# Optimization experiments

Measured on AMD Instinct MI355X. Metric: run time of the kernel, lower is better.

Reference implementation:

```python
import jax, jax.numpy as jnp
import numpy as np

SH_C0 = 0.28209479177387814
EPS2D = 0.3      # gsplat low-pass filter added to 2D covariance diagonal
NEAR = 0.01
ALPHA_MIN = 1.0 / 255.0
ALPHA_MAX = 0.999


def setup_inputs() -> dict:
    key = jax.random.key(0)
    ks = jax.random.split(key, 5)
    N = 2048
    means = 0.1 * jax.random.normal(ks[0], (N, 3), jnp.float32)
    quats = jax.random.normal(ks[1], (N, 4), jnp.float32)
    scales = -2.3 + 0.3 * jax.random.normal(ks[2], (N, 3), jnp.float32)
    opacities = -1.0 + 0.5 * jax.random.normal(ks[3], (N,), jnp.float32)
    sh_coeffs = jax.random.normal(ks[4], (N, 1, 3), jnp.float32)
    viewmats = jnp.eye(4, dtype=jnp.float32).at[2, 3].set(2.0)[None]  # [1,4,4] world->cam
    Ks = jnp.array([[[150.0, 0.0, 64.0], [0.0, 150.0, 64.0], [0.0, 0.0, 1.0]]], jnp.float32)
    return dict(means=means, quats=quats, scales=scales, opacities=opacities,
                sh_coeffs=sh_coeffs, viewmats=viewmats, Ks=Ks, width=128, height=128)


def _splat_render(means, quats, scales, opacities, sh_coeffs, viewmats, Ks, width, height):
    # --- parameter activations (GaussianSplat.activated_parameters) ---
    quats = quats / jnp.linalg.norm(quats, axis=-1, keepdims=True)
    scales = jnp.minimum(jnp.exp(scales), 10.0)
    opac = jax.nn.sigmoid(opacities)                                  # [N]
    colors = jnp.maximum(sh_coeffs[:, 0, :] * SH_C0 + 0.5, 0.0)       # [N,3] sh_degree=0

    # --- 3D covariance from quaternion (w,x,y,z) and scale ---
    w, x, y, z = quats[:, 0], quats[:, 1], quats[:, 2], quats[:, 3]
    R = jnp.stack([
        1 - 2 * (y * y + z * z), 2 * (x * y - w * z), 2 * (x * z + w * y),
        2 * (x * y + w * z), 1 - 2 * (x * x + z * z), 2 * (y * z - w * x),
        2 * (x * z - w * y), 2 * (y * z + w * x), 1 - 2 * (x * x + y * y)],
        axis=-1).reshape(-1, 3, 3)                                    # [N,3,3]
    M = R * scales[:, None, :]                                        # R @ diag(s)
    cov3d = jnp.einsum('nij,nkj->nik', M, M)                          # [N,3,3]

    # --- project to camera frame ---
    Rcw = viewmats[:, :3, :3]                                         # [C,3,3]
    tcw = viewmats[:, :3, 3]                                          # [C,3]
    p_cam = jnp.einsum('cij,nj->cni', Rcw, means) + tcw[:, None, :]   # [C,N,3]
    Vc = jnp.einsum('cij,njk,clk->cnil', Rcw, cov3d, Rcw)             # [C,N,3,3]

    xc, yc, zc = p_cam[..., 0], p_cam[..., 1], p_cam[..., 2]
    valid = zc > NEAR
    zs = jnp.where(valid, zc, 1.0)
    rz = 1.0 / zs
    fx = Ks[:, 0, 0][:, None]; fy = Ks[:, 1, 1][:, None]
    cx = Ks[:, 0, 2][:, None]; cy = Ks[:, 1, 2][:, None]
    u = fx * xc * rz + cx                                             # [C,N]
    v = fy * yc * rz + cy

    # --- EWA 2D covariance: J Vc J^T + eps2d*I, J = d(proj)/d(p_cam) ---
    J00 = fx * rz; J02 = -fx * xc * rz * rz
    J11 = fy * rz; J12 = -fy * yc * rz * rz
    V00, V01, V02 = Vc[..., 0, 0], Vc[..., 0, 1], Vc[..., 0, 2]
    V11, V12, V22 = Vc[..., 1, 1], Vc[..., 1, 2], Vc[..., 2, 2]
    a = J00 * J00 * V00 + 2 * J00 * J02 * V02 + J02 * J02 * V22 + EPS2D
    b = J00 * (J11 * V01 + J12 * V02) + J02 * (J11 * V12 + J12 * V22)
    c = J11 * J11 * V11 + 2 * J11 * J12 * V12 + J12 * J12 * V22 + EPS2D
    det = a * c - b * b
    valid = valid & (det > 0)
    det_s = jnp.where(valid, det, 1.0)
    conA = c / det_s; conB = -b / det_s; conC = a / det_s             # conic (inverse cov)

    # --- per-pixel gaussian evaluation (pixel centers at +0.5) ---
    px = jnp.arange(width, dtype=jnp.float32) + 0.5                   # [W]
    py = jnp.arange(height, dtype=jnp.float32) + 0.5                  # [H]
    dx = px[None, None, :] - u[..., None]                             # [C,N,W]
    dy = py[None, None, :] - v[..., None]                             # [C,N,H]
    sigma = (0.5 * (conA[..., None, None] * (dx * dx)[:, :, None, :]
                    + conC[..., None, None] * (dy * dy)[..., None])
             + conB[..., None, None] * dy[..., None] * dx[:, :, None, :])  # [C,N,H,W]
    alpha = opac[None, :, None, None] * jnp.exp(-sigma)
    alpha = jnp.minimum(alpha, ALPHA_MAX)
    alpha = jnp.where(valid[..., None, None] & (alpha >= ALPHA_MIN), alpha, 0.0)

    # --- front-to-back alpha compositing in depth order ---
    order = jnp.argsort(jnp.where(valid, zc, jnp.inf), axis=1)        # [C,N]
    alpha_s = jnp.take_along_axis(alpha, order[:, :, None, None], axis=1)
    colors_s = jnp.take_along_axis(jnp.broadcast_to(colors[None], (alpha.shape[0],) + colors.shape),
                                   order[:, :, None], axis=1)         # [C,N,3]
    logT = jnp.cumsum(jnp.log1p(-alpha_s), axis=1)
    logT_excl = jnp.pad(logT, ((0, 0), (1, 0), (0, 0), (0, 0)))[:, :-1]
    weights = alpha_s * jnp.exp(logT_excl)                            # [C,N,H,W]
    img = jnp.einsum('cnhw,cnk->chwk', weights, colors_s)             # [C,H,W,3]
    return img


def reference(means, quats, scales, opacities, sh_coeffs, viewmats, Ks, width, height):
    return _splat_render(means, quats, scales, opacities, sh_coeffs, viewmats, Ks, width, height)
```

## Files before the change

kernel.cpp:

```cpp
#include <hip/hip_runtime.h>
#include <math.h>

#define SH_C0     0.28209479177387814f
#define EPS2D     0.3f
#define NEARZ     0.01f
#define ALPHA_MIN (1.0f/255.0f)
#define ALPHA_MAX 0.999f
#define LOG2E     1.4426950408889634f

#define NSEG   16
#define MAXN   2048

__global__ __launch_bounds__(256) void prep_rank_kernel(
        const float* __restrict__ means,
        const float* __restrict__ quats,
        const float* __restrict__ scales,
        const float* __restrict__ opacities,
        const float* __restrict__ sh,
        const float* __restrict__ vm,
        const float* __restrict__ K,
        float* __restrict__ rec,
        float* __restrict__ bbox,
        int N) {
    int wave = blockIdx.x * 4 + (threadIdx.x >> 6);
    int lane = threadIdx.x & 63;
    if (wave >= N) return;
    int i = wave;

    float r00=vm[0], r01=vm[1], r02=vm[2],  t0=vm[3];
    float r10=vm[4], r11=vm[5], r12=vm[6],  t1=vm[7];
    float r20=vm[8], r21=vm[9], r22=vm[10], t2=vm[11];

    float mx = means[3*i+0], my = means[3*i+1], mz = means[3*i+2];
    float zci = r20*mx + r21*my + r22*mz + t2;
    float keyi = (zci > NEARZ) ? zci : INFINITY;
    int cnt = 0;
    for (int j = lane; j < N; j += 64) {
        float ax = means[3*j+0], ay = means[3*j+1], az = means[3*j+2];
        float zcj = r20*ax + r21*ay + r22*az + t2;
        float keyj = (zcj > NEARZ) ? zcj : INFINITY;
        cnt += (keyj < keyi) || (keyj == keyi && j < i);
    }
    #pragma unroll
    for (int off = 32; off > 0; off >>= 1)
        cnt += __shfl_xor(cnt, off, 64);

    float qw = quats[4*i+0], qx = quats[4*i+1], qy = quats[4*i+2], qz = quats[4*i+3];
    float rqn = rsqrtf(qw*qw + qx*qx + qy*qy + qz*qz);
    qw *= rqn; qx *= rqn; qy *= rqn; qz *= rqn;

    float R00 = 1.f - 2.f*(qy*qy + qz*qz);
    float R01 = 2.f*(qx*qy - qw*qz);
    float R02 = 2.f*(qx*qz + qw*qy);
    float R10 = 2.f*(qx*qy + qw*qz);
    float R11 = 1.f - 2.f*(qx*qx + qz*qz);
    float R12 = 2.f*(qy*qz - qw*qx);
    float R20 = 2.f*(qx*qz - qw*qy);
    float R21 = 2.f*(qy*qz + qw*qx);
    float R22 = 1.f - 2.f*(qx*qx + qy*qy);

    float s0 = fminf(expf(scales[3*i+0]), 10.f);
    float s1 = fminf(expf(scales[3*i+1]), 10.f);
    float s2 = fminf(expf(scales[3*i+2]), 10.f);

    float M00=R00*s0, M01=R01*s1, M02=R02*s2;
    float M10=R10*s0, M11=R11*s1, M12=R12*s2;
    float M20=R20*s0, M21=R21*s1, M22=R22*s2;

    float c00 = M00*M00 + M01*M01 + M02*M02;
    float c01 = M00*M10 + M01*M11 + M02*M12;
    float c02 = M00*M20 + M01*M21 + M02*M22;
    float c11 = M10*M10 + M11*M11 + M12*M12;
    float c12 = M10*M20 + M11*M21 + M12*M22;
    float c22 = M20*M20 + M21*M21 + M22*M22;

    float xc = r00*mx + r01*my + r02*mz + t0;
    float yc = r10*mx + r11*my + r12*mz + t1;
    float zc = zci;

    float T00 = r00*c00 + r01*c01 + r02*c02;
    float T01 = r00*c01 + r01*c11 + r02*c12;
    float T02 = r00*c02 + r01*c12 + r02*c22;
    float T10 = r10*c00 + r11*c01 + r12*c02;
    float T11 = r10*c01 + r11*c11 + r12*c12;
    float T12 = r10*c02 + r11*c12 + r12*c22;
    float T20 = r20*c00 + r21*c01 + r22*c02;
    float T21 = r20*c01 + r21*c11 + r22*c12;
    float T22 = r20*c02 + r21*c12 + r22*c22;
    float V00 = T00*r00 + T01*r01 + T02*r02;
    float V01 = T00*r10 + T01*r11 + T02*r12;
    float V02 = T00*r20 + T01*r21 + T02*r22;
    float V11 = T10*r10 + T11*r11 + T12*r12;
    float V12 = T10*r20 + T11*r21 + T12*r22;
    float V22 = T20*r20 + T21*r21 + T22*r22;

    float fx = K[0], cx = K[2], fy = K[4], cy = K[5];

    bool valid = zc > NEARZ;
    float zs = valid ? zc : 1.0f;
    float rz = 1.0f / zs;
    float u = fx*xc*rz + cx;
    float v = fy*yc*rz + cy;
    float J00 = fx*rz;
    float J02 = -fx*xc*rz*rz;
    float J11 = fy*rz;
    float J12 = -fy*yc*rz*rz;

    float a = J00*J00*V00 + 2.f*J00*J02*V02 + J02*J02*V22 + EPS2D;
    float b = J00*(J11*V01 + J12*V02) + J02*(J11*V12 + J12*V22);
    float c = J11*J11*V11 + 2.f*J11*J12*V12 + J12*J12*V22 + EPS2D;
    float det = a*c - b*b;
    valid = valid && (det > 0.f);
    float det_s = valid ? det : 1.0f;
    float conA =  c / det_s;
    float conB = -b / det_s;
    float conC =  a / det_s;

    float op  = 1.0f / (1.0f + expf(-opacities[i]));
    float cr = fmaxf(sh[3*i+0]*SH_C0 + 0.5f, 0.f);
    float cg = fmaxf(sh[3*i+1]*SH_C0 + 0.5f, 0.f);
    float cb = fmaxf(sh[3*i+2]*SH_C0 + 0.5f, 0.f);

    float smax = logf(op * 255.0f);
    bool vis = valid && (smax > 0.f);
    float denom = conA*conC - conB*conB;
    float uu = -1.0e9f, vv = -1.0e9f;
    float rxp = 0.f, ryp = 0.f;
    float e2 = 0.f, e3 = 0.f, e4 = 0.f, e5 = -1.0e4f;
    if (vis) {
        float inv = 2.f * smax / denom;
        rxp = sqrtf(fmaxf(inv * conC, 0.f)) + 4.0f;
        ryp = sqrtf(fmaxf(inv * conA, 0.f)) + 4.0f;
        uu = u; vv = v;
        e2 = 0.5f*conA*LOG2E; e3 = conB*LOG2E; e4 = 0.5f*conC*LOG2E;
        e5 = log2f(op);
    }

    if (lane < 16) {
        float val;
        switch (lane) {
            case 0:  val = uu;  break;
            case 1:  val = vv;  break;
            case 2:  val = e2;  break;
            case 3:  val = e3;  break;
            case 4:  val = e4;  break;
            case 5:  val = e5;  break;
            case 6:  val = cr;  break;
            case 7:  val = cg;  break;
            case 8:  val = cb;  break;
            case 9:  val = 0.f; break;
            case 10: val = 0.f; break;
            case 11: val = 0.f; break;
            case 12: val = uu;  break;
            case 13: val = vv;  break;
            case 14: val = rxp; break;
            default: val = ryp; break;
        }
        if (lane < 12) rec[12*(size_t)cnt + lane] = val;
        else           bbox[4*(size_t)cnt + (lane - 12)] = val;
    }
}

__global__ __launch_bounds__(1024, 4) void render_tile_kernel(
        const float4* __restrict__ rec,
        const float4* __restrict__ bbox,
        float* __restrict__ out,
        int N) {
    __shared__ unsigned long long masks[(MAXN + 63) / 64];
    __shared__ int cnts[NSEG];
    __shared__ unsigned short list[MAXN];
    __shared__ float4 part[NSEG][64];

    int tid  = threadIdx.x;
    int lane = tid & 63;
    int w    = tid >> 6;
    int t    = blockIdx.x;
    int tx   = (t & 15) << 3;
    int ty   = (t >> 4) << 3;

    float tcx = (float)tx + 4.0f;
    float tcy = (float)ty + 4.0f;
    float px  = (float)(tx + (lane & 7)) + 0.5f;
    float py  = (float)(ty + (lane >> 3)) + 0.5f;

    int nwords = (N + 63) >> 6;
    int wpw    = (nwords + NSEG - 1) / NSEG;
    int w0     = w * wpw;
    int w1     = min(w0 + wpw, nwords);

    int mycnt = 0;
    for (int word = w0; word < w1; ++word) {
        int g = (word << 6) + lane;
        bool hit = false;
        if (g < N) {
            float4 bb = bbox[g];
            hit = (fabsf(bb.x - tcx) <= bb.z) &&
                  (fabsf(bb.y - tcy) <= bb.w);
        }
        unsigned long long m = __ballot(hit);
        if (lane == 0) masks[word] = m;
        mycnt += (int)__popcll(m);
    }
    if (lane == 0) cnts[w] = mycnt;
    __syncthreads();

    int off = 0, L = 0;
    #pragma unroll
    for (int s = 0; s < NSEG; ++s) {
        int cs = cnts[s];
        if (s < w) off += cs;
        L += cs;
    }
    unsigned long long lt = (1ull << lane) - 1ull;
    for (int word = w0; word < w1; ++word) {
        unsigned long long m = masks[word];
        bool hit = (m >> lane) & 1ull;
        int p = (int)__popcll(m & lt);
        if (hit) list[off + p] = (unsigned short)((word << 6) + lane);
        off += (int)__popcll(m);
    }
    __syncthreads();

    int chunk = (L + NSEG - 1) / NSEG;
    int i0 = min(w * chunk, L);
    int i1 = min(i0 + chunk, L);

    float accr = 0.f, accg = 0.f, accb = 0.f, T = 1.f;
    #pragma unroll 2
    for (int i = i0; i < i1; ++i) {
        int idx = __builtin_amdgcn_readfirstlane((int)list[i]);
        const float4* r = rec + 3*(size_t)idx;
        float4 r0 = r[0];
        float4 r1 = r[1];
        float4 r2 = r[2];
        float dx = px - r0.x, dy = py - r0.y;
        float tt  = fmaf(r0.z, dx, r0.w * dy);
        float arg = fmaf(-r1.x, dy*dy, r1.y);
        arg = fmaf(-dx, tt, arg);
        float al  = __builtin_amdgcn_exp2f(arg);
        al = fminf(al, ALPHA_MAX);
        al = (al >= ALPHA_MIN) ? al : 0.f;
        float wg = T * al;
        accr = fmaf(wg, r1.z, accr);
        accg = fmaf(wg, r1.w, accg);
        accb = fmaf(wg, r2.x, accb);
        T = fmaf(-al, T, T);
    }
    part[w][lane] = make_float4(accr, accg, accb, T);
    __syncthreads();

    if (tid < 64) {
        float R = 0.f, G = 0.f, B = 0.f, Tr = 1.f;
        #pragma unroll
        for (int s = 0; s < NSEG; ++s) {
            float4 q = part[s][tid];
            R  = fmaf(Tr, q.x, R);
            G  = fmaf(Tr, q.y, G);
            B  = fmaf(Tr, q.z, B);
            Tr *= q.w;
        }
        int x = tx + (tid & 7);
        int y = ty + (tid >> 3);
        int p = y * 128 + x;
        out[3*(size_t)p+0] = R;
        out[3*(size_t)p+1] = G;
        out[3*(size_t)p+2] = B;
    }
}

extern "C" void kernel_launch(void* const* d_in, const int* in_sizes, int n_in,
                              void* d_out, int out_size, void* d_ws, size_t ws_size,
                              hipStream_t stream) {
    const float* means     = (const float*)d_in[0];
    const float* quats     = (const float*)d_in[1];
    const float* scales    = (const float*)d_in[2];
    const float* opacities = (const float*)d_in[3];
    const float* sh        = (const float*)d_in[4];
    const float* vm        = (const float*)d_in[5];
    const float* K         = (const float*)d_in[6];

    int N = in_sizes[0] / 3;

    float* rec  = (float*)d_ws;
    float* bbox = rec + (size_t)N * 12;

    prep_rank_kernel<<<(N + 3) / 4, 256, 0, stream>>>(
        means, quats, scales, opacities, sh, vm, K, rec, bbox, N);
    render_tile_kernel<<<256, 1024, 0, stream>>>(
        (const float4*)rec, (const float4*)bbox, (float*)d_out, N);
}
```

Measured before the change: 108.5 us.

## Split binning into separate kernel writing per-tile contiguous gaussian records

Moves per-tile culling into a new bin_kernel that gathers each hit gaussian's 48-byte record into a contiguous per-tile buffer in workspace. The render kernel then streams records sequentially instead of doing an indirect lookup through a shared-memory index list. This aims to remove the dependent index load and scattered gathers from the compositing loop. In exchange it adds a kernel launch and a large amount of global memory traffic (up to 256*N*48 bytes of workspace), and it needs that much workspace to be available.

New measurement: 112.3 us. 3.5% more time.

```diff
diff --git a/kernel.cpp b/kernel.cpp
--- a/kernel.cpp
+++ b/kernel.cpp
@@ -161,30 +161,24 @@
     }
 }
 
-__global__ __launch_bounds__(1024, 4) void render_tile_kernel(
+__global__ __launch_bounds__(256) void bin_kernel(
         const float4* __restrict__ rec,
         const float4* __restrict__ bbox,
-        float* __restrict__ out,
+        float4* __restrict__ tiles,
+        int* __restrict__ counts,
         int N) {
     __shared__ unsigned long long masks[(MAXN + 63) / 64];
-    __shared__ int cnts[NSEG];
-    __shared__ unsigned short list[MAXN];
-    __shared__ float4 part[NSEG][64];
+    __shared__ int cnts[4];
 
     int tid  = threadIdx.x;
     int lane = tid & 63;
     int w    = tid >> 6;
     int t    = blockIdx.x;
-    int tx   = (t & 15) << 3;
-    int ty   = (t >> 4) << 3;
-
-    float tcx = (float)tx + 4.0f;
-    float tcy = (float)ty + 4.0f;
-    float px  = (float)(tx + (lane & 7)) + 0.5f;
-    float py  = (float)(ty + (lane >> 3)) + 0.5f;
+    float tcx = (float)((t & 15) << 3) + 4.0f;
+    float tcy = (float)((t >> 4) << 3) + 4.0f;
 
     int nwords = (N + 63) >> 6;
-    int wpw    = (nwords + NSEG - 1) / NSEG;
+    int wpw    = (nwords + 3) >> 2;
     int w0     = w * wpw;
     int w1     = min(w0 + wpw, nwords);
 
@@ -206,30 +200,57 @@
 
     int off = 0, L = 0;
     #pragma unroll
-    for (int s = 0; s < NSEG; ++s) {
+    for (int s = 0; s < 4; ++s) {
         int cs = cnts[s];
         if (s < w) off += cs;
         L += cs;
     }
+    float4* tbase = tiles + (size_t)t * N * 3;
     unsigned long long lt = (1ull << lane) - 1ull;
     for (int word = w0; word < w1; ++word) {
         unsigned long long m = masks[word];
         bool hit = (m >> lane) & 1ull;
         int p = (int)__popcll(m & lt);
-        if (hit) list[off + p] = (unsigned short)((word << 6) + lane);
+        if (hit) {
+            int g = (word << 6) + lane;
+            float4 a = rec[3*(size_t)g + 0];
+            float4 b = rec[3*(size_t)g + 1];
+            float4 c = rec[3*(size_t)g + 2];
+            float4* dst = tbase + 3*(size_t)(off + p);
+            dst[0] = a; dst[1] = b; dst[2] = c;
+        }
         off += (int)__popcll(m);
     }
-    __syncthreads();
-
+    if (tid == 0) counts[t] = L;
+}
+
+__global__ __launch_bounds__(1024) void render_tile_kernel(
+        const float4* __restrict__ tiles,
+        const int* __restrict__ counts,
+        float* __restrict__ out,
+        int N) {
+    __shared__ float4 part[NSEG][64];
+
+    int tid  = threadIdx.x;
+    int lane = tid & 63;
+    int w    = __builtin_amdgcn_readfirstlane(tid >> 6);
+    int t    = blockIdx.x;
+    int tx   = (t & 15) << 3;
+    int ty   = (t >> 4) << 3;
+
+    float px = (float)(tx + (lane & 7)) + 0.5f;
+    float py = (float)(ty + (lane >> 3)) + 0.5f;
+
+    int L = counts[t];
     int chunk = (L + NSEG - 1) / NSEG;
     int i0 = min(w * chunk, L);
     int i1 = min(i0 + chunk, L);
 
+    const float4* r = tiles + ((size_t)t * N + i0) * 3;
+
     float accr = 0.f, accg = 0.f, accb = 0.f, T = 1.f;
     #pragma unroll 2
-    for (int i = i0; i < i1; ++i) {
-        int idx = __builtin_amdgcn_readfirstlane((int)list[i]);
-        const float4* r = rec + 3*(size_t)idx;
+    for (int i = i0; i < i1; ++i, r += 3) {
         float4 r0 = r[0];
         float4 r1 = r[1];
         float4 r2 = r[2];
@@ -281,11 +302,16 @@
 
     int N = in_sizes[0] / 3;
 
-    float* rec  = (float*)d_ws;
-    float* bbox = rec + (size_t)N * 12;
+    char* ws = (char*)d_ws;
+    float* rec    = (float*)ws;
+    float* bbox   = (float*)(ws + (size_t)N * 48);
+    float4* tiles = (float4*)(ws + (size_t)N * 64);
+    int*   counts = (int*)(ws + (size_t)N * 64 + (size_t)256 * N * 48);
 
     prep_rank_kernel<<<(N + 3) / 4, 256, 0, stream>>>(
         means, quats, scales, opacities, sh, vm, K, rec, bbox, N);
+    bin_kernel<<<256, 256, 0, stream>>>(
+        (const float4*)rec, (const float4*)bbox, tiles, counts, N);
     render_tile_kernel<<<256, 1024, 0, stream>>>(
-        (const float4*)rec, (const float4*)bbox, (float*)d_out, N);
+        (const float4*)tiles, counts, (float*)d_out, N);
 }
```
